# Optimization experiments

Measured on AMD Instinct MI355X. Metric: run time of the kernel, lower is better.

Reference implementation:

```python
import jax, jax.numpy as jnp
import numpy as np

P = 256          # planes == in_planes
EPS = 1e-5       # BatchNorm eps


def binarize(x):
    # sign with sign(0) -> +1, as in standard binary-net quantizers
    return jnp.where(x >= 0, 1.0, -1.0).astype(x.dtype)


def bin_conv(x, w, stride=1):
    """XNOR-style binarized 3x3 conv: sign(x) * sign(w), scaled by per-out-channel mean |w|."""
    ba = binarize(x)
    bw = binarize(w)
    scale = jnp.mean(jnp.abs(w), axis=(1, 2, 3))  # [O]
    y = jax.lax.conv_general_dilated(
        ba, bw, window_strides=(stride, stride), padding=((1, 1), (1, 1)),
        dimension_numbers=("NCHW", "OIHW", "NCHW"))
    return y * scale[None, :, None, None]


def bn(x, gamma, beta, mean, var):
    # inference-mode BatchNorm2d
    inv = gamma / jnp.sqrt(var + EPS)
    return x * inv[None, :, None, None] + (beta - mean * inv)[None, :, None, None]


def channel_shuffle(x, groups=2):
    b, c, h, w = x.shape
    return x.reshape(b, groups, c // groups, h, w).transpose(0, 2, 1, 3, 4).reshape(b, c, h, w)


def setup_inputs() -> dict:
    key = jax.random.key(0)
    ks = jax.random.split(key, 8)
    B, H, W = 16, 56, 56
    return {
        "x": jax.random.normal(ks[0], (B, 2 * P, H, W), jnp.float32),
        "w1": jax.random.normal(ks[1], (P, P, 3, 3), jnp.float32) * 0.05,
        "w2": jax.random.normal(ks[2], (P, 2 * P, 3, 3), jnp.float32) * 0.05,
        "gamma1": jnp.ones((P,), jnp.float32),
        "beta1": jnp.zeros((P,), jnp.float32),
        "mean1": jax.random.normal(ks[3], (P,), jnp.float32) * 0.1,
        "var1": jax.random.uniform(ks[4], (P,), jnp.float32) + 0.5,
        "gamma2": jnp.ones((P,), jnp.float32),
        "beta2": jnp.zeros((P,), jnp.float32),
        "mean2": jax.random.normal(ks[5], (P,), jnp.float32) * 0.1,
        "var2": jax.random.uniform(ks[6], (P,), jnp.float32) + 0.5,
        "move_bias": jax.random.normal(ks[7], (1, P, 1, 1), jnp.float32) * 0.1,
    }


def reference(x, w1, w2, gamma1, beta1, mean1, var1,
              gamma2, beta2, mean2, var2, move_bias):
    x_act, x_idle = x[:, :P], x[:, P:]
    residual = x_act
    out = bn(bin_conv(x_act, w1, stride=1), gamma1, beta1, mean1, var1)
    out = out + residual
    out = jnp.clip(out, -1.0, 1.0)            # Hardtanh
    x_idle = x_idle + move_bias               # LearnableBias
    out = jnp.concatenate([out, x_idle], axis=1)   # [B, 2P, H, W]
    out = channel_shuffle(out, groups=2)
    residual1 = out[:, :P]
    out = bn(bin_conv(out, w2, stride=1), gamma2, beta2, mean2, var2)
    out = out + residual1
    out = jnp.clip(out, -1.0, 1.0)            # Hardtanh
    return out
```

## Files before the change

### kernel.cpp

```cpp
#include <hip/hip_runtime.h>
#include <cstdint>

typedef unsigned long long u64;

#define HWSZ 3136
#define WD 56
#define NPIX 50176
#define NB 16

__device__ __forceinline__ float clampf(float v){ return fminf(1.0f, fmaxf(-1.0f, v)); }

__global__ __launch_bounds__(256) void k_wprep(
    const float* __restrict__ w1, const float* __restrict__ w2,
    const float* __restrict__ g1, const float* __restrict__ be1,
    const float* __restrict__ m1, const float* __restrict__ v1,
    const float* __restrict__ g2, const float* __restrict__ be2,
    const float* __restrict__ m2, const float* __restrict__ v2,
    u64* __restrict__ w1b, u64* __restrict__ w2e, u64* __restrict__ w2o,
    float* __restrict__ A1, float* __restrict__ B1,
    float* __restrict__ A2, float* __restrict__ B2)
{
    int co  = blockIdx.x;
    int tid = threadIdx.x;
    int wv = tid >> 6, lane = tid & 63;
    int ci = (wv << 6) + lane;

    float s1 = 0.f, s2 = 0.f;
    const float* w1p = w1 + ((size_t)co * 256 + ci) * 9;
#pragma unroll
    for (int t = 0; t < 9; t++) {
        float v = w1p[t];
        s1 += fabsf(v);
        u64 bal = __ballot(v >= 0.f);
        if (lane == 0) w1b[(co * 9 + t) * 4 + wv] = bal;
    }
    const float* wep = w2 + ((size_t)co * 512 + 2 * ci) * 9;
    const float* wop = wep + 9;
#pragma unroll
    for (int t = 0; t < 9; t++) {
        float ve = wep[t], vo = wop[t];
        s2 += fabsf(ve) + fabsf(vo);
        u64 bale = __ballot(ve >= 0.f);
        u64 balo = __ballot(vo >= 0.f);
        if (lane == 0) { w2e[(co * 9 + t) * 4 + wv] = bale; w2o[(co * 9 + t) * 4 + wv] = balo; }
    }
    __shared__ float red1[256], red2[256];
    red1[tid] = s1; red2[tid] = s2;
    __syncthreads();
    for (int off = 128; off > 0; off >>= 1) {
        if (tid < off) { red1[tid] += red1[tid + off]; red2[tid] += red2[tid + off]; }
        __syncthreads();
    }
    if (tid == 0) {
        float scale1 = red1[0] / 2304.f;
        float scale2 = red2[0] / 4608.f;
        float inv1 = g1[co] / sqrtf(v1[co] + 1e-5f);
        float inv2 = g2[co] / sqrtf(v2[co] + 1e-5f);
        A1[co] = scale1 * inv1;  B1[co] = be1[co] - m1[co] * inv1;
        A2[co] = scale2 * inv2;  B2[co] = be2[co] - m2[co] * inv2;
    }
}

__global__ __launch_bounds__(256) void k_pack(
    const float* __restrict__ x, const float* __restrict__ mb,
    u64* __restrict__ bitsA, u64* __restrict__ bitsI)
{
    int tid = threadIdx.x;
    int p = blockIdx.x * 256 + tid;
    int q = blockIdx.y;
    int b = p / HWSZ, hw = p % HWSZ;
    const float* xa = x + ((size_t)(b * 512 + q * 64)) * HWSZ + hw;
    const float* xi = x + ((size_t)(b * 512 + 256 + q * 64)) * HWSZ + hw;
    const float* mbq = mb + q * 64;
    u64 wa = 0, wi = 0;
#pragma unroll 8
    for (int j = 0; j < 64; j++) {
        float va = xa[(size_t)j * HWSZ];
        float vi = xi[(size_t)j * HWSZ] + mbq[j];
        wa |= (u64)(va >= 0.f) << j;
        wi |= (u64)(vi >= 0.f) << j;
    }
    bitsA[(size_t)p * 4 + q] = wa;
    bitsI[(size_t)p * 4 + q] = wi;
}

__global__ __launch_bounds__(256) void k_conv1(
    const float* __restrict__ x, const u64* __restrict__ bitsA,
    const u64* __restrict__ w1b, const float* __restrict__ A1, const float* __restrict__ B1,
    u64* __restrict__ bitsC, float* __restrict__ c1v)
{
    __shared__ u64 sw[2304];
    __shared__ float sA[64], sB[64];
    int tid = threadIdx.x;
    int q = blockIdx.y;
    int cobase = q * 64;
    {
        const u64* src = w1b + (size_t)cobase * 36;
#pragma unroll
        for (int i = 0; i < 9; i++) sw[tid + i * 256] = src[tid + i * 256];
        if (tid < 64) { sA[tid] = A1[cobase + tid]; sB[tid] = B1[cobase + tid]; }
    }
    __syncthreads();

    int p = blockIdx.x * 256 + tid;
    int b = p / HWSZ, hw = p % HWSZ;
    int h = hw / WD, w = hw % WD;

    int acc[64];
#pragma unroll
    for (int i = 0; i < 64; i++) acc[i] = 0;
    int nvalid = 0;
#pragma unroll 1
    for (int t = 0; t < 9; t++) {
        int dy = t / 3 - 1, dx = t % 3 - 1;
        int hh = h + dy, ww = w + dx;
        bool valid = (hh >= 0 && hh < WD && ww >= 0 && ww < WD);
        u64 n0 = 0, n1 = 0, n2 = 0, n3 = 0;
        if (valid) {
            const u64* nb = bitsA + (size_t)(p + dy * WD + dx) * 4;
            n0 = nb[0]; n1 = nb[1]; n2 = nb[2]; n3 = nb[3];
        }
        int mask = valid ? -1 : 0;
        nvalid -= mask;
#pragma unroll
        for (int co = 0; co < 64; co++) {
            const u64* wp = &sw[(co * 9 + t) * 4];
            int pt = __popcll(n0 ^ wp[0]) + __popcll(n1 ^ wp[1])
                   + __popcll(n2 ^ wp[2]) + __popcll(n3 ^ wp[3]);
            acc[co] += pt & mask;
        }
    }
    u64 signw = 0;
    const float* xr = x + ((size_t)(b * 512 + cobase)) * HWSZ + hw;
    float* cv = c1v + (size_t)cobase * NPIX + p;
#pragma unroll
    for (int co = 0; co < 64; co++) {
        int y = (nvalid << 8) - 2 * acc[co];
        float v = (float)y * sA[co] + sB[co] + xr[(size_t)co * HWSZ];
        signw |= (u64)(v >= 0.f) << co;
        if (q < 2) cv[(size_t)co * NPIX] = clampf(v);
    }
    bitsC[(size_t)p * 4 + q] = signw;
}

__global__ __launch_bounds__(256) void k_conv2(
    const float* __restrict__ x, const float* __restrict__ mb,
    const u64* __restrict__ bitsC, const u64* __restrict__ bitsI,
    const u64* __restrict__ w2e, const u64* __restrict__ w2o,
    const float* __restrict__ A2, const float* __restrict__ B2,
    const float* __restrict__ c1v, float* __restrict__ out)
{
    __shared__ u64 se[2304], so[2304];
    __shared__ float sA[64], sB[64], sM[32];
    int tid = threadIdx.x;
    int q = blockIdx.y;
    int cobase = q * 64;
    {
        const u64* srcE = w2e + (size_t)cobase * 36;
        const u64* srcO = w2o + (size_t)cobase * 36;
#pragma unroll
        for (int i = 0; i < 9; i++) { se[tid + i * 256] = srcE[tid + i * 256]; so[tid + i * 256] = srcO[tid + i * 256]; }
        if (tid < 64) { sA[tid] = A2[cobase + tid]; sB[tid] = B2[cobase + tid]; }
        if (tid < 32) { sM[tid] = mb[cobase / 2 + tid]; }
    }
    __syncthreads();

    int p = blockIdx.x * 256 + tid;
    int b = p / HWSZ, hw = p % HWSZ;
    int h = hw / WD, w = hw % WD;

    int acc[64];
#pragma unroll
    for (int i = 0; i < 64; i++) acc[i] = 0;
    int nvalid = 0;
#pragma unroll 1
    for (int t = 0; t < 9; t++) {
        int dy = t / 3 - 1, dx = t % 3 - 1;
        int hh = h + dy, ww = w + dx;
        bool valid = (hh >= 0 && hh < WD && ww >= 0 && ww < WD);
        u64 c0 = 0, c1 = 0, c2 = 0, c3 = 0, i0 = 0, i1 = 0, i2 = 0, i3 = 0;
        if (valid) {
            size_t np = (size_t)(p + dy * WD + dx) * 4;
            c0 = bitsC[np]; c1 = bitsC[np + 1]; c2 = bitsC[np + 2]; c3 = bitsC[np + 3];
            i0 = bitsI[np]; i1 = bitsI[np + 1]; i2 = bitsI[np + 2]; i3 = bitsI[np + 3];
        }
        int mask = valid ? -1 : 0;
        nvalid -= mask;
#pragma unroll
        for (int co = 0; co < 64; co++) {
            const u64* we = &se[(co * 9 + t) * 4];
            const u64* wo = &so[(co * 9 + t) * 4];
            int pt = __popcll(c0 ^ we[0]) + __popcll(c1 ^ we[1])
                   + __popcll(c2 ^ we[2]) + __popcll(c3 ^ we[3])
                   + __popcll(i0 ^ wo[0]) + __popcll(i1 ^ wo[1])
                   + __popcll(i2 ^ wo[2]) + __popcll(i3 ^ wo[3]);
            acc[co] += pt & mask;
        }
    }
    const float* xo = x + ((size_t)(b * 512 + 256 + 32 * q)) * HWSZ + hw;
    const float* cvr = c1v + (size_t)(32 * q) * NPIX + p;
    float* op = out + ((size_t)(b * 256 + cobase)) * HWSZ + hw;
#pragma unroll
    for (int co = 0; co < 64; co++) {
        int y = (nvalid << 9) - 2 * acc[co];
        float v = (float)y * sA[co] + sB[co];
        int cg2 = co >> 1;
        float res;
        if ((co & 1) == 0) res = cvr[(size_t)cg2 * NPIX];
        else               res = xo[(size_t)cg2 * HWSZ] + sM[cg2];
        v += res;
        op[(size_t)co * HWSZ] = clampf(v);
    }
}

extern "C" void kernel_launch(void* const* d_in, const int* in_sizes, int n_in,
                              void* d_out, int out_size, void* d_ws, size_t ws_size,
                              hipStream_t stream)
{
    const float* x   = (const float*)d_in[0];
    const float* w1  = (const float*)d_in[1];
    const float* w2  = (const float*)d_in[2];
    const float* g1  = (const float*)d_in[3];
    const float* be1 = (const float*)d_in[4];
    const float* m1  = (const float*)d_in[5];
    const float* v1  = (const float*)d_in[6];
    const float* g2  = (const float*)d_in[7];
    const float* be2 = (const float*)d_in[8];
    const float* m2  = (const float*)d_in[9];
    const float* v2  = (const float*)d_in[10];
    const float* mb  = (const float*)d_in[11];

    char* ws = (char*)d_ws;
    u64* w1b = (u64*)ws; ws += 73728;
    u64* w2e = (u64*)ws; ws += 73728;
    u64* w2o = (u64*)ws; ws += 73728;
    float* A1 = (float*)ws; ws += 1024;
    float* B1 = (float*)ws; ws += 1024;
    float* A2 = (float*)ws; ws += 1024;
    float* B2 = (float*)ws; ws += 1024;
    u64* bitsA = (u64*)ws; ws += (size_t)NPIX * 4 * 8;
    u64* bitsI = (u64*)ws; ws += (size_t)NPIX * 4 * 8;
    u64* bitsC = (u64*)ws; ws += (size_t)NPIX * 4 * 8;
    float* c1v = (float*)ws; ws += (size_t)128 * NPIX * 4;

    hipLaunchKernelGGL(k_wprep, dim3(256), dim3(256), 0, stream,
                       w1, w2, g1, be1, m1, v1, g2, be2, m2, v2,
                       w1b, w2e, w2o, A1, B1, A2, B2);
    hipLaunchKernelGGL(k_pack, dim3(196, 4), dim3(256), 0, stream, x, mb, bitsA, bitsI);
    hipLaunchKernelGGL(k_conv1, dim3(196, 4), dim3(256), 0, stream,
                       x, bitsA, w1b, A1, B1, bitsC, c1v);
    hipLaunchKernelGGL(k_conv2, dim3(196, 4), dim3(256), 0, stream,
                       x, mb, bitsC, bitsI, w2e, w2o, A2, B2, c1v, (float*)d_out);
}
```

Before: 462.0 us.

## Retile binary convs to 2 pixels x 16 channels per thread with row reuse

Both popcount conv kernels now give each thread two adjacent pixels and 16 output channels instead of one pixel and 64 channels. A block's four wavefronts split the 64 channels, and the grid doubles. Each weight word read from shared memory is now used for two pixels, neighbour bit loads are shared across the 3 dx taps of a row, and residual/output accesses use float2. The accumulator array drops from 64 to 32 registers to raise occupancy. In conv1 the per-wave 16-bit sign fragments are combined through shared memory, which adds a barrier, and the per-thread channel count is smaller, so each neighbour load feeds less arithmetic.

```diff
diff --git a/kernel.cpp b/kernel.cpp
--- a/kernel.cpp
+++ b/kernel.cpp
@@ -2,11 +2,11 @@
 #include <cstdint>
 
 typedef unsigned long long u64;
+typedef unsigned short u16;
 
 #define HWSZ 3136
 #define WD 56
 #define NPIX 50176
-#define NB 16
 
 __device__ __forceinline__ float clampf(float v){ return fminf(1.0f, fmaxf(-1.0f, v)); }
 
@@ -84,13 +84,14 @@
     bitsI[(size_t)p * 4 + q] = wi;
 }
 
-__global__ __launch_bounds__(256) void k_conv1(
+__global__ __launch_bounds__(256, 4) void k_conv1(
     const float* __restrict__ x, const u64* __restrict__ bitsA,
     const u64* __restrict__ w1b, const float* __restrict__ A1, const float* __restrict__ B1,
     u64* __restrict__ bitsC, float* __restrict__ c1v)
 {
     __shared__ u64 sw[2304];
     __shared__ float sA[64], sB[64];
+    __shared__ u16 spart[4][128];
     int tid = threadIdx.x;
     int q = blockIdx.y;
     int cobase = q * 64;
@@ -102,48 +103,83 @@
     }
     __syncthreads();
 
-    int p = blockIdx.x * 256 + tid;
-    int b = p / HWSZ, hw = p % HWSZ;
+    int g = tid >> 6, lane = tid & 63;
+    int pix0 = blockIdx.x * 128 + lane * 2;
+    int b = pix0 / HWSZ, hw = pix0 % HWSZ;
     int h = hw / WD, w = hw % WD;
 
-    int acc[64];
-#pragma unroll
-    for (int i = 0; i < 64; i++) acc[i] = 0;
-    int nvalid = 0;
+    int acc[16][2];
+#pragma unroll
+    for (int co = 0; co < 16; co++) { acc[co][0] = 0; acc[co][1] = 0; }
+    int nv0 = 0, nv1 = 0;
+
 #pragma unroll 1
-    for (int t = 0; t < 9; t++) {
-        int dy = t / 3 - 1, dx = t % 3 - 1;
-        int hh = h + dy, ww = w + dx;
-        bool valid = (hh >= 0 && hh < WD && ww >= 0 && ww < WD);
-        u64 n0 = 0, n1 = 0, n2 = 0, n3 = 0;
-        if (valid) {
-            const u64* nb = bitsA + (size_t)(p + dy * WD + dx) * 4;
-            n0 = nb[0]; n1 = nb[1]; n2 = nb[2]; n3 = nb[3];
-        }
-        int mask = valid ? -1 : 0;
-        nvalid -= mask;
-#pragma unroll
-        for (int co = 0; co < 64; co++) {
-            const u64* wp = &sw[(co * 9 + t) * 4];
-            int pt = __popcll(n0 ^ wp[0]) + __popcll(n1 ^ wp[1])
-                   + __popcll(n2 ^ wp[2]) + __popcll(n3 ^ wp[3]);
-            acc[co] += pt & mask;
-        }
-    }
-    u64 signw = 0;
-    const float* xr = x + ((size_t)(b * 512 + cobase)) * HWSZ + hw;
-    float* cv = c1v + (size_t)cobase * NPIX + p;
-#pragma unroll
-    for (int co = 0; co < 64; co++) {
-        int y = (nvalid << 8) - 2 * acc[co];
-        float v = (float)y * sA[co] + sB[co] + xr[(size_t)co * HWSZ];
-        signw |= (u64)(v >= 0.f) << co;
-        if (q < 2) cv[(size_t)co * NPIX] = clampf(v);
-    }
-    bitsC[(size_t)p * 4 + q] = signw;
-}
-
-__global__ __launch_bounds__(256) void k_conv2(
+    for (int dy = -1; dy <= 1; dy++) {
+        bool rowok = ((unsigned)(h + dy)) < (unsigned)WD;
+        u64 cb[4][4];
+        int m[4];
+#pragma unroll
+        for (int k = 0; k < 4; k++) {
+            int c = w - 1 + k;
+            bool ok = rowok && ((unsigned)c < (unsigned)WD);
+            int pg = pix0 + dy * WD + (k - 1);
+            pg = pg < 0 ? 0 : (pg > NPIX - 1 ? NPIX - 1 : pg);
+            const ulonglong2* pb = (const ulonglong2*)(bitsA + (size_t)pg * 4);
+            ulonglong2 b01 = pb[0], b23 = pb[1];
+            cb[k][0] = b01.x; cb[k][1] = b01.y; cb[k][2] = b23.x; cb[k][3] = b23.y;
+            m[k] = ok ? -1 : 0;
+        }
+        int tbase = (dy + 1) * 3;
+#pragma unroll
+        for (int dx = 0; dx < 3; dx++) {
+            int t = tbase + dx;
+            nv0 -= m[dx]; nv1 -= m[dx + 1];
+#pragma unroll
+            for (int co = 0; co < 16; co++) {
+                const u64* wp = &sw[(((g << 4) + co) * 9 + t) * 4];
+                u64 w0 = wp[0], w1_ = wp[1], w2_ = wp[2], w3_ = wp[3];
+#pragma unroll
+                for (int p = 0; p < 2; p++) {
+                    int k = dx + p;
+                    int pt = __popcll(cb[k][0] ^ w0) + __popcll(cb[k][1] ^ w1_)
+                           + __popcll(cb[k][2] ^ w2_) + __popcll(cb[k][3] ^ w3_);
+                    acc[co][p] += pt & m[k];
+                }
+            }
+        }
+    }
+
+    unsigned sb0 = 0, sb1 = 0;
+    bool wr = (q < 2);
+#pragma unroll
+    for (int co = 0; co < 16; co++) {
+        int col = (g << 4) + co;
+        int coG = cobase + col;
+        float A = sA[col], B = sB[col];
+        float2 xr = *(const float2*)(x + (size_t)(b * 512 + coG) * HWSZ + hw);
+        float v0 = (float)((nv0 << 8) - 2 * acc[co][0]) * A + B + xr.x;
+        float v1 = (float)((nv1 << 8) - 2 * acc[co][1]) * A + B + xr.y;
+        sb0 |= (unsigned)(v0 >= 0.f) << co;
+        sb1 |= (unsigned)(v1 >= 0.f) << co;
+        if (wr) {
+            *(float2*)(c1v + (size_t)coG * NPIX + pix0) = make_float2(clampf(v0), clampf(v1));
+        }
+    }
+    spart[g][lane * 2]     = (u16)sb0;
+    spart[g][lane * 2 + 1] = (u16)sb1;
+    __syncthreads();
+    if (g == 0) {
+#pragma unroll
+        for (int p = 0; p < 2; p++) {
+            int pi = lane * 2 + p;
+            u64 word = (u64)spart[0][pi] | ((u64)spart[1][pi] << 16)
+                     | ((u64)spart[2][pi] << 32) | ((u64)spart[3][pi] << 48);
+            bitsC[(size_t)(pix0 + p) * 4 + q] = word;
+        }
+    }
+}
+
+__global__ __launch_bounds__(256, 3) void k_conv2(
     const float* __restrict__ x, const float* __restrict__ mb,
     const u64* __restrict__ bitsC, const u64* __restrict__ bitsI,
     const u64* __restrict__ w2e, const u64* __restrict__ w2o,
@@ -161,55 +197,82 @@
 #pragma unroll
         for (int i = 0; i < 9; i++) { se[tid + i * 256] = srcE[tid + i * 256]; so[tid + i * 256] = srcO[tid + i * 256]; }
         if (tid < 64) { sA[tid] = A2[cobase + tid]; sB[tid] = B2[cobase + tid]; }
-        if (tid < 32) { sM[tid] = mb[cobase / 2 + tid]; }
+        if (tid < 32) { sM[tid] = mb[q * 32 + tid]; }
     }
     __syncthreads();
 
-    int p = blockIdx.x * 256 + tid;
-    int b = p / HWSZ, hw = p % HWSZ;
+    int g = tid >> 6, lane = tid & 63;
+    int pix0 = blockIdx.x * 128 + lane * 2;
+    int b = pix0 / HWSZ, hw = pix0 % HWSZ;
     int h = hw / WD, w = hw % WD;
 
-    int acc[64];
-#pragma unroll
-    for (int i = 0; i < 64; i++) acc[i] = 0;
-    int nvalid = 0;
+    int acc[16][2];
+#pragma unroll
+    for (int co = 0; co < 16; co++) { acc[co][0] = 0; acc[co][1] = 0; }
+    int nv0 = 0, nv1 = 0;
+
 #pragma unroll 1
-    for (int t = 0; t < 9; t++) {
-        int dy = t / 3 - 1, dx = t % 3 - 1;
-        int hh = h + dy, ww = w + dx;
-        bool valid = (hh >= 0 && hh < WD && ww >= 0 && ww < WD);
-        u64 c0 = 0, c1 = 0, c2 = 0, c3 = 0, i0 = 0, i1 = 0, i2 = 0, i3 = 0;
-        if (valid) {
-            size_t np = (size_t)(p + dy * WD + dx) * 4;
-            c0 = bitsC[np]; c1 = bitsC[np + 1]; c2 = bitsC[np + 2]; c3 = bitsC[np + 3];
-            i0 = bitsI[np]; i1 = bitsI[np + 1]; i2 = bitsI[np + 2]; i3 = bitsI[np + 3];
-        }
-        int mask = valid ? -1 : 0;
-        nvalid -= mask;
-#pragma unroll
-        for (int co = 0; co < 64; co++) {
-            const u64* we = &se[(co * 9 + t) * 4];
-            const u64* wo = &so[(co * 9 + t) * 4];
-            int pt = __popcll(c0 ^ we[0]) + __popcll(c1 ^ we[1])
-                   + __popcll(c2 ^ we[2]) + __popcll(c3 ^ we[3])
-                   + __popcll(i0 ^ wo[0]) + __popcll(i1 ^ wo[1])
-                   + __popcll(i2 ^ wo[2]) + __popcll(i3 ^ wo[3]);
-            acc[co] += pt & mask;
-        }
-    }
-    const float* xo = x + ((size_t)(b * 512 + 256 + 32 * q)) * HWSZ + hw;
-    const float* cvr = c1v + (size_t)(32 * q) * NPIX + p;
-    float* op = out + ((size_t)(b * 256 + cobase)) * HWSZ + hw;
-#pragma unroll
-    for (int co = 0; co < 64; co++) {
-        int y = (nvalid << 9) - 2 * acc[co];
-        float v = (float)y * sA[co] + sB[co];
-        int cg2 = co >> 1;
-        float res;
-        if ((co & 1) == 0) res = cvr[(size_t)cg2 * NPIX];
-        else               res = xo[(size_t)cg2 * HWSZ] + sM[cg2];
-        v += res;
-        op[(size_t)co * HWSZ] = clampf(v);
+    for (int dy = -1; dy <= 1; dy++) {
+        bool rowok = ((unsigned)(h + dy)) < (unsigned)WD;
+        u64 cb[4][4], ib[4][4];
+        int m[4];
+#pragma unroll
+        for (int k = 0; k < 4; k++) {
+            int c = w - 1 + k;
+            bool ok = rowok && ((unsigned)c < (unsigned)WD);
+            int pg = pix0 + dy * WD + (k - 1);
+            pg = pg < 0 ? 0 : (pg > NPIX - 1 ? NPIX - 1 : pg);
+            const ulonglong2* pc = (const ulonglong2*)(bitsC + (size_t)pg * 4);
+            const ulonglong2* pi = (const ulonglong2*)(bitsI + (size_t)pg * 4);
+            ulonglong2 c01 = pc[0], c23 = pc[1];
+            ulonglong2 i01 = pi[0], i23 = pi[1];
+            cb[k][0] = c01.x; cb[k][1] = c01.y; cb[k][2] = c23.x; cb[k][3] = c23.y;
+            ib[k][0] = i01.x; ib[k][1] = i01.y; ib[k][2] = i23.x; ib[k][3] = i23.y;
+            m[k] = ok ? -1 : 0;
+        }
+        int tbase = (dy + 1) * 3;
+#pragma unroll
+        for (int dx = 0; dx < 3; dx++) {
+            int t = tbase + dx;
+            nv0 -= m[dx]; nv1 -= m[dx + 1];
+#pragma unroll
+            for (int co = 0; co < 16; co++) {
+                const u64* we = &se[(((g << 4) + co) * 9 + t) * 4];
+                const u64* wo = &so[(((g << 4) + co) * 9 + t) * 4];
+                u64 e0 = we[0], e1 = we[1], e2 = we[2], e3 = we[3];
+                u64 o0 = wo[0], o1 = wo[1], o2 = wo[2], o3 = wo[3];
+#pragma unroll
+                for (int p = 0; p < 2; p++) {
+                    int k = dx + p;
+                    int pt = __popcll(cb[k][0] ^ e0) + __popcll(cb[k][1] ^ e1)
+                           + __popcll(cb[k][2] ^ e2) + __popcll(cb[k][3] ^ e3)
+                           + __popcll(ib[k][0] ^ o0) + __popcll(ib[k][1] ^ o1)
+                           + __popcll(ib[k][2] ^ o2) + __popcll(ib[k][3] ^ o3);
+                    acc[co][p] += pt & m[k];
+                }
+            }
+        }
+    }
+
+#pragma unroll
+    for (int co = 0; co < 16; co++) {
+        int col = (g << 4) + co;
+        int coG = cobase + col;
+        int cg2 = coG >> 1;
+        float A = sA[col], B = sB[col];
+        float v0 = (float)((nv0 << 9) - 2 * acc[co][0]) * A + B;
+        float v1 = (float)((nv1 << 9) - 2 * acc[co][1]) * A + B;
+        float r0, r1;
+        if ((co & 1) == 0) {
+            float2 cv = *(const float2*)(c1v + (size_t)cg2 * NPIX + pix0);
+            r0 = cv.x; r1 = cv.y;
+        } else {
+            float2 xi = *(const float2*)(x + (size_t)(b * 512 + 256 + cg2) * HWSZ + hw);
+            float mbv = sM[col >> 1];
+            r0 = xi.x + mbv; r1 = xi.y + mbv;
+        }
+        *(float2*)(out + (size_t)(b * 256 + coG) * HWSZ + hw) =
+            make_float2(clampf(v0 + r0), clampf(v1 + r1));
     }
 }
 
@@ -247,8 +310,8 @@
                        w1, w2, g1, be1, m1, v1, g2, be2, m2, v2,
                        w1b, w2e, w2o, A1, B1, A2, B2);
     hipLaunchKernelGGL(k_pack, dim3(196, 4), dim3(256), 0, stream, x, mb, bitsA, bitsI);
-    hipLaunchKernelGGL(k_conv1, dim3(196, 4), dim3(256), 0, stream,
+    hipLaunchKernelGGL(k_conv1, dim3(392, 4), dim3(256), 0, stream,
                        x, bitsA, w1b, A1, B1, bitsC, c1v);
-    hipLaunchKernelGGL(k_conv2, dim3(196, 4), dim3(256), 0, stream,
+    hipLaunchKernelGGL(k_conv2, dim3(392, 4), dim3(256), 0, stream,
                        x, mb, bitsC, bitsI, w2e, w2o, A2, B2, c1v, (float*)d_out);
 }
```

Result: faster. 409.8 us (-11.3%).
